# Kernel tuning notes

Measured on AMD Instinct MI355X. Metric: run time of the kernel, lower is better.

## Reference

```python
import jax, jax.numpy as jnp
import numpy as np


def topk_sparsify(x, k):
    # keep k entries with largest |x|, zero the rest (matches TopKFunction.forward)
    _, idx = jax.lax.top_k(jnp.abs(x), k)            # [B, k]
    vals = jnp.take_along_axis(x, idx, axis=-1)      # [B, k]
    out = jnp.zeros_like(x)
    b = jnp.arange(x.shape[0])[:, None]              # [B, 1]
    return out.at[b, idx].set(vals)


def setup_inputs() -> dict:
    key = jax.random.key(0)
    k1, k2, k3 = jax.random.split(key, 3)
    B, D, L = 4096, 768, 16384
    x = jax.random.normal(k1, (B, D), dtype=jnp.float32)
    # kaiming_normal_(fan_out) -> std = sqrt(2 / latent_dim); then *= 2.0
    enc_w = jax.random.normal(k2, (L, D), dtype=jnp.float32) * (2.0 * np.sqrt(2.0 / L))
    enc_b = jnp.zeros((L,), dtype=jnp.float32)
    # torch Linear default init: uniform(-1/sqrt(fan_in), 1/sqrt(fan_in))
    bound = 1.0 / np.sqrt(L)
    dec_w = jax.random.uniform(k3, (D, L), dtype=jnp.float32, minval=-bound, maxval=bound)
    dec_b = jnp.zeros((D,), dtype=jnp.float32)
    return {"x": x, "enc_w": enc_w, "enc_b": enc_b, "dec_w": dec_w, "dec_b": dec_b, "k": 32}


def reference(x, enc_w, enc_b, dec_w, dec_b, k):
    pre = x @ enc_w.T + enc_b            # [B, L]
    latents = topk_sparsify(pre, k)      # [B, L], k-sparse per row
    recon = latents @ dec_w.T + dec_b    # [B, D]
    return (recon, latents, pre)
```

## Files before the change

kernel.cpp:

```cpp
#include <hip/hip_runtime.h>
#include <hip/hip_bf16.h>
#include <stdint.h>


typedef __attribute__((ext_vector_type(8))) short bf16x8;
typedef __attribute__((ext_vector_type(4))) float f32x4;

__device__ __forceinline__ ushort f2bf_rne(float v) {
    unsigned u = __float_as_uint(v);
    return (ushort)((u + 0x7fffu + ((u >> 16) & 1u)) >> 16);
}
__device__ __forceinline__ float bf2f(ushort h) {
    return __uint_as_float(((unsigned)h) << 16);
}

__global__ __launch_bounds__(256)
void pack_bf16(const float* __restrict__ X, ushort* __restrict__ Ph,
               int R16KT, int KT, int K)
{
    int t = blockIdx.x * 256 + threadIdx.x;
    if (t >= R16KT * 64) return;
    int lane = t & 63;
    int rest = t >> 6;
    int r16 = rest / KT, kt = rest - r16 * KT;
    int row = (r16 << 4) + (lane & 15);
    int k0  = (kt << 5) + ((lane >> 4) << 3);
    const float* src = X + (size_t)row * K + k0;

    uint hw[4];
    #pragma unroll
    for (int i = 0; i < 4; ++i) {
        float v0 = src[2 * i], v1 = src[2 * i + 1];
        hw[i] = (uint)f2bf_rne(v0) | ((uint)f2bf_rne(v1) << 16);
    }
    *reinterpret_cast<uint4*>(Ph + (size_t)t * 8) = make_uint4(hw[0], hw[1], hw[2], hw[3]);
}

__global__ __launch_bounds__(256, 2)
void encoder_mfma1(const ushort* __restrict__ Ah, const ushort* __restrict__ Wh,
                   const float* __restrict__ bias, float* __restrict__ C,
                   int M, int N, int K)
{
    __shared__ ushort lds[8192];
    const int KT = K >> 5;
    const int tid  = threadIdx.x;
    const int lane = tid & 63;
    const int wid  = tid >> 6;

    int nwg  = gridDim.x;
    int flat = blockIdx.x;
    int cpx  = nwg >> 3;
    int swz  = (flat & 7) * cpx + (flat >> 3);
    const int gx = N >> 7;
    const int bx = swz % gx, by = swz / gx;

    const int wr = wid >> 1, wc = wid & 1;

    f32x4 acc[4][4];
    #pragma unroll
    for (int m = 0; m < 4; ++m)
        #pragma unroll
        for (int n = 0; n < 4; ++n) acc[m][n] = (f32x4){0.f, 0.f, 0.f, 0.f};

    for (int kt = 0; kt < KT; ++kt) {
        #pragma unroll
        for (int c0 = 0; c0 < 4; ++c0) {
            int c   = (wid << 2) + c0;
            int fr  = c & 7;
            int rb  = ((c < 8) ? (by << 3) : (bx << 3)) + fr;
            const ushort* g = ((c < 8) ? Ah : Wh) + (((size_t)rb * KT + kt) * 64 + lane) * 8;
            ushort* dst = &lds[c * 512];
            __builtin_amdgcn_global_load_lds(
                (const __attribute__((address_space(1))) unsigned int*)g,
                (__attribute__((address_space(3))) unsigned int*)dst, 16, 0, 0);
        }
        __syncthreads();

        bf16x8 ah[4], bh[4];
        #pragma unroll
        for (int m = 0; m < 4; ++m)
            ah[m] = *reinterpret_cast<const bf16x8*>(&lds[((wr << 2) + m) * 512 + lane * 8]);
        #pragma unroll
        for (int n = 0; n < 4; ++n)
            bh[n] = *reinterpret_cast<const bf16x8*>(&lds[4096 + ((wc << 2) + n) * 512 + lane * 8]);

        #pragma unroll
        for (int m = 0; m < 4; ++m)
            #pragma unroll
            for (int n = 0; n < 4; ++n)
                acc[m][n] = __builtin_amdgcn_mfma_f32_16x16x32_bf16(ah[m], bh[n], acc[m][n], 0, 0, 0);
        __syncthreads();
    }

    const int r_in = (lane >> 4) << 2;
    const int c_in = lane & 15;
    #pragma unroll
    for (int n = 0; n < 4; ++n) {
        const int gc = (bx << 7) + (wc << 6) + (n << 4) + c_in;
        const float bv = bias[gc];
        #pragma unroll
        for (int m = 0; m < 4; ++m) {
            const int gr0 = (by << 7) + (wr << 6) + (m << 4) + r_in;
            #pragma unroll
            for (int q = 0; q < 4; ++q)
                C[(size_t)(gr0 + q) * N + gc] = acc[m][n][q] + bv;
        }
    }
}

#define SR_CAP 1024
#define SR_ZCAP 128

__global__ __launch_bounds__(256, 8)
void select_refine(const float* __restrict__ pre, const float* __restrict__ x,
                   const float* __restrict__ enc_w, const float* __restrict__ enc_b,
                   float* __restrict__ latents, int* __restrict__ sel_idx,
                   float* __restrict__ sel_val, const int* __restrict__ kptr,
                   int D, int L)
{
    const int b   = blockIdx.x;
    const int tid = threadIdx.x;
    const float* row = pre + (size_t)b * L;
    float* lrow = latents + (size_t)b * L;

    __shared__ float    xs[768];
    __shared__ float    smp[256];
    __shared__ float    sthr[3];
    __shared__ int      cnt;
    __shared__ unsigned long long lkey[SR_CAP];
    __shared__ float    lval[SR_CAP];
    __shared__ float    s_tk;
    __shared__ float    s_xn2;
    __shared__ int      zidx[SR_ZCAP];
    __shared__ float    zval[SR_ZCAP];
    __shared__ int      zn;
    __shared__ int      fin_n;
    __shared__ int      fin_i[64];
    __shared__ float    fin_v[64];
    __shared__ float    red[4];

    int k = *kptr; if (k > 64) k = 64; if (k < 1) k = 1;

    float xn2p = 0.f;
    for (int i = tid; i < D; i += 256) {
        float v = x[(size_t)b * D + i];
        xs[i] = v;
        xn2p = fmaf(v, v, xn2p);
    }
    #pragma unroll
    for (int off = 32; off > 0; off >>= 1) xn2p += __shfl_down(xn2p, off);
    if ((tid & 63) == 0) red[tid >> 6] = xn2p;
    if (tid == 0) { zn = 0; fin_n = 0; }
    __syncthreads();
    if (tid == 0) s_xn2 = red[0] + red[1] + red[2] + red[3];

    const int stride = L >> 8;
    smp[tid] = fabsf(row[(size_t)tid * stride]);
    __syncthreads();
    {
        float s = smp[tid];
        int r = 0;
        for (int j = 0; j < 256; ++j) {
            float o = smp[j];
            r += (o > s || (o == s && j < tid)) ? 1 : 0;
        }
        if (r == 1) sthr[0] = s;
        if (r == 3) sthr[1] = s;
        if (r == 7) sthr[2] = s;
    }
    __syncthreads();

    float t = sthr[1];
    int n = 0;
    for (int attempt = 0; attempt < 2; ++attempt) {
        __syncthreads();
        if (tid == 0) cnt = 0;
        __syncthreads();
        for (int i = tid * 4; i < L; i += 1024) {
            float4 v = *reinterpret_cast<const float4*>(row + i);
            float vv[4] = {v.x, v.y, v.z, v.w};
            #pragma unroll
            for (int j = 0; j < 4; ++j) {
                float av = fabsf(vv[j]);
                if (av >= t) {
                    int p = atomicAdd(&cnt, 1);
                    if (p < SR_CAP) {
                        lkey[p] = ((unsigned long long)__float_as_uint(av) << 32)
                                  | (unsigned)(~(i + j));
                        lval[p] = vv[j];
                    }
                }
            }
        }
        __syncthreads();
        n = cnt;
        if (n >= 48 && n <= SR_CAP) break;
        t = (n < 48) ? sthr[2] : sthr[0];
    }
    if (n > SR_CAP) n = SR_CAP;
    if (k > n) k = n;

    const float4 z4 = make_float4(0.f, 0.f, 0.f, 0.f);
    for (int i = tid * 4; i < L; i += 1024)
        *reinterpret_cast<float4*>(lrow + i) = z4;

    for (int i = tid; i < n; i += 256) {
        unsigned long long ki = lkey[i];
        int rk = 0;
        for (int j = 0; j < n; ++j) rk += (lkey[j] > ki) ? 1 : 0;
        if (rk == k - 1) s_tk = fabsf(lval[i]);
    }
    __syncthreads();

    const float tk = s_tk;
    const float m  = 1.2e-3f * sqrtf(s_xn2);

    for (int i = tid; i < n; i += 256) {
        float a = fabsf(lval[i]);
        if (a > tk + m) {
            int p = atomicAdd(&fin_n, 1);
            fin_i[p] = (int)(~(unsigned)lkey[i]);
            fin_v[p] = lval[i];
        } else if (a >= tk - m) {
            int zp = atomicAdd(&zn, 1);
            if (zp < SR_ZCAP) zidx[zp] = (int)(~(unsigned)lkey[i]);
        }
    }
    __syncthreads();
    const int A  = fin_n;
    const int nz = (zn < SR_ZCAP) ? zn : SR_ZCAP;

    for (int z = 0; z < nz; ++z) {
        const int l = zidx[z];
        const float* wrow = enc_w + (size_t)l * D;
        float s = 0.f;
        for (int d = tid; d < D; d += 256) s = fmaf(xs[d], wrow[d], s);
        #pragma unroll
        for (int off = 32; off > 0; off >>= 1) s += __shfl_down(s, off);
        if ((tid & 63) == 0) red[tid >> 6] = s;
        __syncthreads();
        if (tid == 0) zval[z] = red[0] + red[1] + red[2] + red[3] + enc_b[l];
        __syncthreads();
    }

    const int k2 = k - A;
    if (tid < nz) {
        float az = fabsf(zval[tid]);
        int   iz = zidx[tid];
        int rz = 0;
        for (int j = 0; j < nz; ++j) {
            float aj = fabsf(zval[j]);
            rz += (aj > az || (aj == az && zidx[j] < iz)) ? 1 : 0;
        }
        if (rz < k2) {
            int p = atomicAdd(&fin_n, 1);
            if (p < 64) { fin_i[p] = iz; fin_v[p] = zval[tid]; }
        }
    }
    __syncthreads();

    int fn = fin_n; if (fn > 64) fn = 64;
    if (tid < fn) {
        float av = fabsf(fin_v[tid]);
        int   ii = fin_i[tid];
        int fr = 0;
        for (int j = 0; j < fn; ++j) {
            float aj = fabsf(fin_v[j]);
            fr += (aj > av || (aj == av && fin_i[j] < ii)) ? 1 : 0;
        }
        sel_idx[(size_t)b * 64 + fr] = ii;
        sel_val[(size_t)b * 64 + fr] = fin_v[tid];
        lrow[ii] = fin_v[tid];
    }
    if (tid >= fn && tid < k) {
        sel_idx[(size_t)b * 64 + tid] = 0;
        sel_val[(size_t)b * 64 + tid] = 0.f;
    }
}

__global__ void transpose_bf16(const float* __restrict__ W, ushort* __restrict__ WT,
                               int D, int L)
{
    __shared__ float tile[32][33];
    const int l0 = blockIdx.x * 32;
    const int d0 = blockIdx.y * 32;
    const int tx = threadIdx.x;
    const int ty = threadIdx.y;
    for (int i = ty; i < 32; i += 8)
        tile[i][tx] = W[(size_t)(d0 + i) * L + (l0 + tx)];
    __syncthreads();
    for (int i = ty; i < 32; i += 8)
        WT[(size_t)(l0 + i) * D + (d0 + tx)] = f2bf_rne(tile[tx][i]);
}

__global__ __launch_bounds__(256)
void decoder_selb(const int* __restrict__ sel_idx, const float* __restrict__ sel_val,
                  const ushort* __restrict__ WT, const float* __restrict__ dbias,
                  float* __restrict__ recon, const int* __restrict__ kptr, int D)
{
    const int b = blockIdx.x;
    const int tid = threadIdx.x;
    int k = *kptr; if (k > 64) k = 64; if (k < 1) k = 1;
    __shared__ int   si[64];
    __shared__ float sv[64];
    if (tid < k) { si[tid] = sel_idx[(size_t)b * 64 + tid]; sv[tid] = sel_val[(size_t)b * 64 + tid]; }
    __syncthreads();
    float a0 = 0.f, a1 = 0.f, a2 = 0.f;
    for (int j = 0; j < k; ++j) {
        const ushort* w = WT + (size_t)si[j] * D;
        const float v = sv[j];
        if (tid < D)        a0 = fmaf(v, bf2f(w[tid]),       a0);
        if (tid + 256 < D)  a1 = fmaf(v, bf2f(w[tid + 256]), a1);
        if (tid + 512 < D)  a2 = fmaf(v, bf2f(w[tid + 512]), a2);
    }
    if (tid < D)       recon[(size_t)b * D + tid]       = a0 + dbias[tid];
    if (tid + 256 < D) recon[(size_t)b * D + tid + 256] = a1 + dbias[tid + 256];
    if (tid + 512 < D) recon[(size_t)b * D + tid + 512] = a2 + dbias[tid + 512];
}

#define BM 128
#define BN 128
#define BKT 16

__global__ __launch_bounds__(256, 2)
void encoder_gemm(const float* __restrict__ A, const float* __restrict__ Bw,
                  const float* __restrict__ bias, float* __restrict__ C,
                  int M, int N, int K)
{
    __shared__ float As[BKT][BM + 4];
    __shared__ float Bs[BKT][BN + 4];
    const int tid  = threadIdx.x;
    const int row0 = blockIdx.y * BM;
    const int col0 = blockIdx.x * BN;
    const int lrow = tid >> 2;
    const int lc4  = (tid & 3) * 4;
    const int ty = tid >> 4;
    const int tx = tid & 15;
    float acc[2][2][4][4];
    #pragma unroll
    for (int a = 0; a < 2; ++a)
        #pragma unroll
        for (int b = 0; b < 2; ++b)
            #pragma unroll
            for (int i = 0; i < 4; ++i)
                #pragma unroll
                for (int j = 0; j < 4; ++j) acc[a][b][i][j] = 0.f;
    for (int k0 = 0; k0 < K; k0 += BKT) {
        float4 a0 = *reinterpret_cast<const float4*>(A + (size_t)(row0 + lrow)      * K + k0 + lc4);
        float4 a1 = *reinterpret_cast<const float4*>(A + (size_t)(row0 + lrow + 64) * K + k0 + lc4);
        float4 b0 = *reinterpret_cast<const float4*>(Bw + (size_t)(col0 + lrow)      * K + k0 + lc4);
        float4 b1 = *reinterpret_cast<const float4*>(Bw + (size_t)(col0 + lrow + 64) * K + k0 + lc4);
        __syncthreads();
        As[lc4 + 0][lrow] = a0.x; As[lc4 + 1][lrow] = a0.y;
        As[lc4 + 2][lrow] = a0.z; As[lc4 + 3][lrow] = a0.w;
        As[lc4 + 0][lrow + 64] = a1.x; As[lc4 + 1][lrow + 64] = a1.y;
        As[lc4 + 2][lrow + 64] = a1.z; As[lc4 + 3][lrow + 64] = a1.w;
        Bs[lc4 + 0][lrow] = b0.x; Bs[lc4 + 1][lrow] = b0.y;
        Bs[lc4 + 2][lrow] = b0.z; Bs[lc4 + 3][lrow] = b0.w;
        Bs[lc4 + 0][lrow + 64] = b1.x; Bs[lc4 + 1][lrow + 64] = b1.y;
        Bs[lc4 + 2][lrow + 64] = b1.z; Bs[lc4 + 3][lrow + 64] = b1.w;
        __syncthreads();
        #pragma unroll
        for (int kk = 0; kk < BKT; ++kk) {
            float av[2][4], bv[2][4];
            *reinterpret_cast<float4*>(av[0]) = *reinterpret_cast<const float4*>(&As[kk][ty * 4]);
            *reinterpret_cast<float4*>(av[1]) = *reinterpret_cast<const float4*>(&As[kk][ty * 4 + 64]);
            *reinterpret_cast<float4*>(bv[0]) = *reinterpret_cast<const float4*>(&Bs[kk][tx * 4]);
            *reinterpret_cast<float4*>(bv[1]) = *reinterpret_cast<const float4*>(&Bs[kk][tx * 4 + 64]);
            #pragma unroll
            for (int a = 0; a < 2; ++a)
                #pragma unroll
                for (int i = 0; i < 4; ++i)
                    #pragma unroll
                    for (int b = 0; b < 2; ++b)
                        #pragma unroll
                        for (int j = 0; j < 4; ++j)
                            acc[a][b][i][j] = fmaf(av[a][i], bv[b][j], acc[a][b][i][j]);
        }
    }
    #pragma unroll
    for (int a = 0; a < 2; ++a)
        #pragma unroll
        for (int i = 0; i < 4; ++i) {
            const int r = row0 + a * 64 + ty * 4 + i;
            #pragma unroll
            for (int b = 0; b < 2; ++b) {
                const int c = col0 + b * 64 + tx * 4;
                float4 o;
                o.x = acc[a][b][i][0] + bias[c + 0];
                o.y = acc[a][b][i][1] + bias[c + 1];
                o.z = acc[a][b][i][2] + bias[c + 2];
                o.w = acc[a][b][i][3] + bias[c + 3];
                *reinterpret_cast<float4*>(C + (size_t)r * N + c) = o;
            }
        }
}

__global__ __launch_bounds__(256)
void topk_kernel(const float* __restrict__ pre, float* __restrict__ latents,
                 const int* __restrict__ kptr, int L)
{
    const int b   = blockIdx.x;
    const int tid = threadIdx.x;
    int k = *kptr; if (k > 64) k = 64; if (k < 1) k = 1;
    const float* row = pre + (size_t)b * L;
    __shared__ unsigned hist[2048];
    __shared__ unsigned coarse[256];
    __shared__ unsigned sh_cgt, sh_prefix;
    __shared__ int      tie_n;
    __shared__ int      tie_idx[1024];
    __shared__ float    tie_val[1024];
    unsigned cgt = 0, prefix = 0;
    for (int level = 0; level < 3; ++level) {
        const int nb     = (level == 0) ? 2048 : 1024;
        const int shift  = (level == 0) ? 20 : (level == 1 ? 10 : 0);
        const int pshift = (level == 1) ? 20 : 10;
        for (int i = tid; i < nb; i += 256) hist[i] = 0;
        __syncthreads();
        for (int i = tid * 4; i < L; i += 1024) {
            float4 v = *reinterpret_cast<const float4*>(row + i);
            float vv[4] = {v.x, v.y, v.z, v.w};
            #pragma unroll
            for (int j = 0; j < 4; ++j) {
                unsigned key = __float_as_uint(vv[j]) & 0x7fffffffu;
                if (level == 0 || (key >> pshift) == prefix)
                    atomicAdd(&hist[(key >> shift) & (nb - 1)], 1u);
            }
        }
        __syncthreads();
        const int per = nb / 256;
        unsigned s = 0;
        for (int j = 0; j < per; ++j) s += hist[tid * per + j];
        coarse[tid] = s;
        __syncthreads();
        if (tid == 0) {
            unsigned run = cgt;
            int bin = 0;
            for (int c = 255; c >= 0; --c) {
                if (run + coarse[c] >= (unsigned)k) {
                    bin = c * per + per - 1;
                    for (; bin > c * per; --bin) {
                        if (run + hist[bin] >= (unsigned)k) break;
                        run += hist[bin];
                    }
                    break;
                }
                run += coarse[c];
            }
            sh_cgt = run;
            sh_prefix = (level == 0) ? (unsigned)bin : ((prefix << 10) | (unsigned)bin);
        }
        __syncthreads();
        cgt = sh_cgt; prefix = sh_prefix;
        __syncthreads();
    }
    const unsigned T = prefix;
    const int r = k - (int)cgt;
    if (tid == 0) tie_n = 0;
    __syncthreads();
    float* lrow = latents + (size_t)b * L;
    for (int i = tid * 4; i < L; i += 1024) {
        float4 v = *reinterpret_cast<const float4*>(row + i);
        float vv[4] = {v.x, v.y, v.z, v.w};
        #pragma unroll
        for (int j = 0; j < 4; ++j) {
            unsigned key = __float_as_uint(vv[j]) & 0x7fffffffu;
            if (key > T) {
                lrow[i + j] = vv[j];
            } else if (key == T) {
                int p = atomicAdd(&tie_n, 1);
                if (p < 1024) { tie_idx[p] = i + j; tie_val[p] = vv[j]; }
            }
        }
    }
    __syncthreads();
    if (tid == 0) {
        int nn = tie_n; if (nn > 1024) nn = 1024;
        for (int a = 1; a < nn; ++a) {
            int ia = tie_idx[a]; float va = tie_val[a];
            int c = a - 1;
            while (c >= 0 && tie_idx[c] > ia) {
                tie_idx[c + 1] = tie_idx[c]; tie_val[c + 1] = tie_val[c]; --c;
            }
            tie_idx[c + 1] = ia; tie_val[c + 1] = va;
        }
        int take = r < nn ? r : nn;
        for (int a = 0; a < take; ++a) lrow[tie_idx[a]] = tie_val[a];
    }
}

__global__ void transpose_kernel(const float* __restrict__ W, float* __restrict__ WT,
                                 int D, int L)
{
    __shared__ float tile[32][33];
    const int l0 = blockIdx.x * 32;
    const int d0 = blockIdx.y * 32;
    const int tx = threadIdx.x;
    const int ty = threadIdx.y;
    for (int i = ty; i < 32; i += 8)
        tile[i][tx] = W[(size_t)(d0 + i) * L + (l0 + tx)];
    __syncthreads();
    for (int i = ty; i < 32; i += 8)
        WT[(size_t)(l0 + i) * D + (d0 + tx)] = tile[tx][i];
}

__global__ __launch_bounds__(256)
void decoder_kernel(const float* __restrict__ latents, const float* __restrict__ WT,
                    const float* __restrict__ Wfall, const float* __restrict__ dbias,
                    float* __restrict__ recon, int L, int D, int useWT)
{
    const int b = blockIdx.x;
    const int tid = threadIdx.x;
    __shared__ int   nsel;
    __shared__ int   s_idx[64];
    __shared__ float s_val[64];
    if (tid == 0) nsel = 0;
    __syncthreads();
    const float* lrow = latents + (size_t)b * L;
    for (int i = tid * 4; i < L; i += 1024) {
        float4 v = *reinterpret_cast<const float4*>(lrow + i);
        float vv[4] = {v.x, v.y, v.z, v.w};
        #pragma unroll
        for (int j = 0; j < 4; ++j) {
            if (vv[j] != 0.0f) {
                int p = atomicAdd(&nsel, 1);
                if (p < 64) { s_idx[p] = i + j; s_val[p] = vv[j]; }
            }
        }
    }
    __syncthreads();
    if (tid == 0) {
        int n = nsel; if (n > 64) n = 64;
        for (int a = 1; a < n; ++a) {
            int ia = s_idx[a]; float va = s_val[a];
            int c = a - 1;
            while (c >= 0 && s_idx[c] > ia) {
                s_idx[c + 1] = s_idx[c]; s_val[c + 1] = s_val[c]; --c;
            }
            s_idx[c + 1] = ia; s_val[c + 1] = va;
        }
    }
    __syncthreads();
    int n = nsel; if (n > 64) n = 64;
    float accv[3] = {0.f, 0.f, 0.f};
    if (useWT) {
        for (int j = 0; j < n; ++j) {
            const int l = s_idx[j]; const float v = s_val[j];
            const float* w = WT + (size_t)l * D;
            #pragma unroll
            for (int c = 0; c < 3; ++c) {
                int d = tid + c * 256;
                if (d < D) accv[c] = fmaf(v, w[d], accv[c]);
            }
        }
    } else {
        for (int j = 0; j < n; ++j) {
            const int l = s_idx[j]; const float v = s_val[j];
            #pragma unroll
            for (int c = 0; c < 3; ++c) {
                int d = tid + c * 256;
                if (d < D) accv[c] = fmaf(v, Wfall[(size_t)d * L + l], accv[c]);
            }
        }
    }
    #pragma unroll
    for (int c = 0; c < 3; ++c) {
        int d = tid + c * 256;
        if (d < D) recon[(size_t)b * D + d] = accv[c] + dbias[d];
    }
}

extern "C" void kernel_launch(void* const* d_in, const int* in_sizes, int n_in,
                              void* d_out, int out_size, void* d_ws, size_t ws_size,
                              hipStream_t stream)
{
    const float* x     = (const float*)d_in[0];
    const float* enc_w = (const float*)d_in[1];
    const float* enc_b = (const float*)d_in[2];
    const float* dec_w = (const float*)d_in[3];
    const float* dec_b = (const float*)d_in[4];
    const int*   kptr  = (const int*)d_in[5];

    const int D = in_sizes[4];
    const int L = in_sizes[2];
    const int B = in_sizes[0] / D;

    float* recon   = (float*)d_out;
    float* latents = recon + (size_t)B * D;
    float* pre     = latents + (size_t)B * L;

    const size_t szA  = (size_t)B * D * 2;
    const size_t szW  = (size_t)L * D * 2;
    const size_t szSel = (size_t)B * 64 * 4;
    size_t off = 0;
    ushort* Ah  = (ushort*)((char*)d_ws + off); off += szA;
    ushort* Wh  = (ushort*)((char*)d_ws + off); off += szW;
    ushort* WTb = (ushort*)((char*)d_ws + off); off += szW;
    int*    sidx = (int*)((char*)d_ws + off);   off += szSel;
    float*  sval = (float*)((char*)d_ws + off); off += szSel;
    const size_t need = off;

    const bool shapes_ok = (B % 128 == 0) && (L % 1024 == 0) && (L >= 2048) &&
                           (D % 32 == 0) && (D <= 768) &&
                           (((size_t)(B / 128) * (L / 128)) % 8 == 0);
    const bool fast = shapes_ok && ws_size >= need;

    if (fast) {
        const int KT = D / 32;
        int totA = (B / 16) * KT * 64;
        pack_bf16<<<(totA + 255) / 256, 256, 0, stream>>>(x, Ah, (B / 16) * KT, KT, D);
        int totW = (L / 16) * KT * 64;
        pack_bf16<<<(totW + 255) / 256, 256, 0, stream>>>(enc_w, Wh, (L / 16) * KT, KT, D);
        transpose_bf16<<<dim3(L / 32, D / 32), dim3(32, 8), 0, stream>>>(dec_w, WTb, D, L);
        encoder_mfma1<<<(B / 128) * (L / 128), 256, 0, stream>>>(Ah, Wh, enc_b, pre, B, L, D);
        select_refine<<<B, 256, 0, stream>>>(pre, x, enc_w, enc_b, latents, sidx, sval, kptr, D, L);
        decoder_selb<<<B, 256, 0, stream>>>(sidx, sval, WTb, dec_b, recon, kptr, D);
    } else {
        hipMemsetAsync(latents, 0, (size_t)B * L * sizeof(float), stream);
        int useWT = 0;
        const size_t szWT = (size_t)L * D * 4;
        if (ws_size >= szWT) {
            useWT = 1;
            transpose_kernel<<<dim3(L / 32, D / 32), dim3(32, 8), 0, stream>>>(dec_w, (float*)d_ws, D, L);
        }
        encoder_gemm<<<dim3(L / BN, B / BM), 256, 0, stream>>>(x, enc_w, enc_b, pre, B, L, D);
        topk_kernel<<<B, 256, 0, stream>>>(pre, latents, kptr, L);
        decoder_kernel<<<B, 256, 0, stream>>>(latents, (float*)d_ws, dec_w, dec_b, recon, L, D, useWT);
    }
}
```

Baseline: 532.9 us.

## Fuse top-k candidate collection and latent zeroing into encoder GEMM epilogue

The encoder epilogue now writes zeros to the latents tile and, for each output whose magnitude exceeds a per-row statistical threshold, appends it to a per-row candidate list via global atomics. The threshold comes from the squared norm of the encoder weights, accumulated in the pack kernel, and the row norm of x. The select kernel reads this small candidate list instead of rescanning the full pre row and zeroing latents itself, falling back to the old sampling scan when the list is too small, too large or the k-th value is too close to the threshold. This removes a full re-read of pre and a separate latents write pass, at the cost of global atomics and scattered writes in the GEMM epilogue plus two extra memsets and a small kernel.

```diff
diff --git a/kernel.cpp b/kernel.cpp
--- a/kernel.cpp
+++ b/kernel.cpp
@@ -6,6 +6,8 @@
 typedef __attribute__((ext_vector_type(8))) short bf16x8;
 typedef __attribute__((ext_vector_type(4))) float f32x4;
 
+#define CAND_CAP 512
+
 __device__ __forceinline__ ushort f2bf_rne(float v) {
     unsigned u = __float_as_uint(v);
     return (ushort)((u + 0x7fffu + ((u >> 16) & 1u)) >> 16);
@@ -16,7 +18,7 @@
 
 __global__ __launch_bounds__(256)
 void pack_bf16(const float* __restrict__ X, ushort* __restrict__ Ph,
-               int R16KT, int KT, int K)
+               float* __restrict__ ss, int R16KT, int KT, int K)
 {
     int t = blockIdx.x * 256 + threadIdx.x;
     if (t >= R16KT * 64) return;
@@ -28,20 +30,45 @@
     const float* src = X + (size_t)row * K + k0;
 
     uint hw[4];
+    float sq = 0.f;
     #pragma unroll
     for (int i = 0; i < 4; ++i) {
         float v0 = src[2 * i], v1 = src[2 * i + 1];
+        sq = fmaf(v0, v0, sq); sq = fmaf(v1, v1, sq);
         hw[i] = (uint)f2bf_rne(v0) | ((uint)f2bf_rne(v1) << 16);
     }
     *reinterpret_cast<uint4*>(Ph + (size_t)t * 8) = make_uint4(hw[0], hw[1], hw[2], hw[3]);
+    if (ss) {
+        #pragma unroll
+        for (int off = 32; off > 0; off >>= 1) sq += __shfl_down(sq, off);
+        if (lane == 0) atomicAdd(ss, sq);
+    }
+}
+
+__global__ __launch_bounds__(256)
+void row_thr(const float* __restrict__ x, const float* __restrict__ ss,
+             float* __restrict__ thr, int D, int LD_total)
+{
+    int row  = blockIdx.x * 4 + (threadIdx.x >> 6);
+    int lane = threadIdx.x & 63;
+    const float* xr = x + (size_t)row * D;
+    float s = 0.f;
+    for (int d = lane; d < D; d += 64) { float v = xr[d]; s = fmaf(v, v, s); }
+    #pragma unroll
+    for (int off = 32; off > 0; off >>= 1) s += __shfl_down(s, off);
+    if (lane == 0)
+        thr[row] = 2.5f * sqrtf(ss[0] / (float)LD_total) * sqrtf(s);
 }
 
 __global__ __launch_bounds__(256, 2)
 void encoder_mfma1(const ushort* __restrict__ Ah, const ushort* __restrict__ Wh,
                    const float* __restrict__ bias, float* __restrict__ C,
+                   float* __restrict__ Lat, uint2* __restrict__ cand,
+                   int* __restrict__ cnt, const float* __restrict__ thr,
                    int M, int N, int K)
 {
     __shared__ ushort lds[8192];
+    __shared__ float  thr_s[128];
     const int KT = K >> 5;
     const int tid  = threadIdx.x;
     const int lane = tid & 63;
@@ -55,6 +82,8 @@
     const int bx = swz % gx, by = swz / gx;
 
     const int wr = wid >> 1, wc = wid & 1;
+
+    if (tid < 128) thr_s[tid] = thr[(by << 7) + tid];
 
     f32x4 acc[4][4];
     #pragma unroll
@@ -100,10 +129,21 @@
         const float bv = bias[gc];
         #pragma unroll
         for (int m = 0; m < 4; ++m) {
-            const int gr0 = (by << 7) + (wr << 6) + (m << 4) + r_in;
+            const int lr0 = (wr << 6) + (m << 4) + r_in;
             #pragma unroll
-            for (int q = 0; q < 4; ++q)
-                C[(size_t)(gr0 + q) * N + gc] = acc[m][n][q] + bv;
+            for (int q = 0; q < 4; ++q) {
+                const int lr = lr0 + q;
+                const int gr = (by << 7) + lr;
+                const float v = acc[m][n][q] + bv;
+                C[(size_t)gr * N + gc]   = v;
+                Lat[(size_t)gr * N + gc] = 0.0f;
+                if (fabsf(v) >= thr_s[lr]) {
+                    int p = atomicAdd(&cnt[gr], 1);
+                    if (p < CAND_CAP)
+                        cand[(size_t)gr * CAND_CAP + p] =
+                            make_uint2((unsigned)gc, __float_as_uint(v));
+                }
+            }
         }
     }
 }
@@ -114,6 +154,8 @@
 __global__ __launch_bounds__(256, 8)
 void select_refine(const float* __restrict__ pre, const float* __restrict__ x,
                    const float* __restrict__ enc_w, const float* __restrict__ enc_b,
+                   const uint2* __restrict__ cand, const int* __restrict__ cnt,
+                   const float* __restrict__ thr,
                    float* __restrict__ latents, int* __restrict__ sel_idx,
                    float* __restrict__ sel_val, const int* __restrict__ kptr,
                    int D, int L)
@@ -126,7 +168,7 @@
     __shared__ float    xs[768];
     __shared__ float    smp[256];
     __shared__ float    sthr[3];
-    __shared__ int      cnt;
+    __shared__ int      scnt;
     __shared__ unsigned long long lkey[SR_CAP];
     __shared__ float    lval[SR_CAP];
     __shared__ float    s_tk;
@@ -154,66 +196,88 @@
     __syncthreads();
     if (tid == 0) s_xn2 = red[0] + red[1] + red[2] + red[3];
 
-    const int stride = L >> 8;
-    smp[tid] = fabsf(row[(size_t)tid * stride]);
-    __syncthreads();
-    {
-        float s = smp[tid];
-        int r = 0;
-        for (int j = 0; j < 256; ++j) {
-            float o = smp[j];
-            r += (o > s || (o == s && j < tid)) ? 1 : 0;
-        }
-        if (r == 1) sthr[0] = s;
-        if (r == 3) sthr[1] = s;
-        if (r == 7) sthr[2] = s;
-    }
-    __syncthreads();
-
-    float t = sthr[1];
+    const int nc = cnt[b];
+    bool usecand = (nc >= k && nc <= CAND_CAP);
     int n = 0;
-    for (int attempt = 0; attempt < 2; ++attempt) {
-        __syncthreads();
-        if (tid == 0) cnt = 0;
-        __syncthreads();
-        for (int i = tid * 4; i < L; i += 1024) {
-            float4 v = *reinterpret_cast<const float4*>(row + i);
-            float vv[4] = {v.x, v.y, v.z, v.w};
-            #pragma unroll
-            for (int j = 0; j < 4; ++j) {
-                float av = fabsf(vv[j]);
-                if (av >= t) {
-                    int p = atomicAdd(&cnt, 1);
-                    if (p < SR_CAP) {
-                        lkey[p] = ((unsigned long long)__float_as_uint(av) << 32)
-                                  | (unsigned)(~(i + j));
-                        lval[p] = vv[j];
+    if (usecand) {
+        for (int i = tid; i < nc; i += 256) {
+            uint2 e = cand[(size_t)b * CAND_CAP + i];
+            lval[i] = __uint_as_float(e.y);
+            lkey[i] = ((unsigned long long)(e.y & 0x7fffffffu) << 32)
+                      | (unsigned)(~e.x);
+        }
+        n = nc;
+    }
+    __syncthreads();
+
+    const float mm   = 1.2e-3f * sqrtf(s_xn2);
+    const float thrb = thr[b];
+    int kk = 0;
+
+    for (int pass = 0; pass < 2; ++pass) {
+        if (!usecand) {
+            const int stride = L >> 8;
+            smp[tid] = fabsf(row[(size_t)tid * stride]);
+            __syncthreads();
+            {
+                float s = smp[tid];
+                int r = 0;
+                for (int j = 0; j < 256; ++j) {
+                    float o = smp[j];
+                    r += (o > s || (o == s && j < tid)) ? 1 : 0;
+                }
+                if (r == 1) sthr[0] = s;
+                if (r == 3) sthr[1] = s;
+                if (r == 7) sthr[2] = s;
+            }
+            __syncthreads();
+            float t = sthr[1];
+            for (int attempt = 0; attempt < 2; ++attempt) {
+                __syncthreads();
+                if (tid == 0) scnt = 0;
+                __syncthreads();
+                for (int i = tid * 4; i < L; i += 1024) {
+                    float4 v = *reinterpret_cast<const float4*>(row + i);
+                    float vv[4] = {v.x, v.y, v.z, v.w};
+                    #pragma unroll
+                    for (int j = 0; j < 4; ++j) {
+                        float av = fabsf(vv[j]);
+                        if (av >= t) {
+                            int p = atomicAdd(&scnt, 1);
+                            if (p < SR_CAP) {
+                                lkey[p] = ((unsigned long long)__float_as_uint(av) << 32)
+                                          | (unsigned)(~(i + j));
+                                lval[p] = vv[j];
+                            }
+                        }
                     }
                 }
-            }
-        }
-        __syncthreads();
-        n = cnt;
-        if (n >= 48 && n <= SR_CAP) break;
-        t = (n < 48) ? sthr[2] : sthr[0];
-    }
-    if (n > SR_CAP) n = SR_CAP;
-    if (k > n) k = n;
-
-    const float4 z4 = make_float4(0.f, 0.f, 0.f, 0.f);
-    for (int i = tid * 4; i < L; i += 1024)
-        *reinterpret_cast<float4*>(lrow + i) = z4;
-
-    for (int i = tid; i < n; i += 256) {
-        unsigned long long ki = lkey[i];
-        int rk = 0;
-        for (int j = 0; j < n; ++j) rk += (lkey[j] > ki) ? 1 : 0;
-        if (rk == k - 1) s_tk = fabsf(lval[i]);
-    }
-    __syncthreads();
-
+                __syncthreads();
+                n = scnt;
+                if (n >= 48 && n <= SR_CAP) break;
+                t = (n < 48) ? sthr[2] : sthr[0];
+            }
+            if (n > SR_CAP) n = SR_CAP;
+        }
+        kk = (k < n) ? k : n;
+
+        if (tid == 0) s_tk = 0.f;
+        __syncthreads();
+        for (int i = tid; i < n; i += 256) {
+            unsigned long long ki = lkey[i];
+            int rk = 0;
+            for (int j = 0; j < n; ++j) rk += (lkey[j] > ki) ? 1 : 0;
+            if (rk == kk - 1) s_tk = fabsf(lval[i]);
+        }
+        __syncthreads();
+
+        if (!usecand) break;
+        if (s_tk >= thrb + 2.0f * mm) break;
+        usecand = false;
+    }
+    k = kk;
     const float tk = s_tk;
-    const float m  = 1.2e-3f * sqrtf(s_xn2);
+    const float m  = mm;
 
     for (int i = tid; i < n; i += 256) {
         float a = fabsf(lval[i]);
@@ -589,15 +653,19 @@
     float* latents = recon + (size_t)B * D;
     float* pre     = latents + (size_t)B * L;
 
-    const size_t szA  = (size_t)B * D * 2;
-    const size_t szW  = (size_t)L * D * 2;
+    const size_t szA   = (size_t)B * D * 2;
+    const size_t szW   = (size_t)L * D * 2;
     const size_t szSel = (size_t)B * 64 * 4;
     size_t off = 0;
-    ushort* Ah  = (ushort*)((char*)d_ws + off); off += szA;
-    ushort* Wh  = (ushort*)((char*)d_ws + off); off += szW;
-    ushort* WTb = (ushort*)((char*)d_ws + off); off += szW;
-    int*    sidx = (int*)((char*)d_ws + off);   off += szSel;
-    float*  sval = (float*)((char*)d_ws + off); off += szSel;
+    ushort* Ah   = (ushort*)((char*)d_ws + off); off += szA;
+    ushort* Wh   = (ushort*)((char*)d_ws + off); off += szW;
+    ushort* WTb  = (ushort*)((char*)d_ws + off); off += szW;
+    int*    sidx = (int*)((char*)d_ws + off);    off += szSel;
+    float*  sval = (float*)((char*)d_ws + off);  off += szSel;
+    uint2*  candb = (uint2*)((char*)d_ws + off); off += (size_t)B * CAND_CAP * 8;
+    int*    cntb  = (int*)((char*)d_ws + off);   off += (size_t)B * 4;
+    float*  thrb  = (float*)((char*)d_ws + off); off += (size_t)B * 4;
+    float*  ssb   = (float*)((char*)d_ws + off); off += 256;
     const size_t need = off;
 
     const bool shapes_ok = (B % 128 == 0) && (L % 1024 == 0) && (L >= 2048) &&
@@ -607,13 +675,18 @@
 
     if (fast) {
         const int KT = D / 32;
+        hipMemsetAsync(cntb, 0, (size_t)B * 4, stream);
+        hipMemsetAsync(ssb, 0, 4, stream);
         int totA = (B / 16) * KT * 64;
-        pack_bf16<<<(totA + 255) / 256, 256, 0, stream>>>(x, Ah, (B / 16) * KT, KT, D);
+        pack_bf16<<<(totA + 255) / 256, 256, 0, stream>>>(x, Ah, nullptr, (B / 16) * KT, KT, D);
         int totW = (L / 16) * KT * 64;
-        pack_bf16<<<(totW + 255) / 256, 256, 0, stream>>>(enc_w, Wh, (L / 16) * KT, KT, D);
+        pack_bf16<<<(totW + 255) / 256, 256, 0, stream>>>(enc_w, Wh, ssb, (L / 16) * KT, KT, D);
         transpose_bf16<<<dim3(L / 32, D / 32), dim3(32, 8), 0, stream>>>(dec_w, WTb, D, L);
-        encoder_mfma1<<<(B / 128) * (L / 128), 256, 0, stream>>>(Ah, Wh, enc_b, pre, B, L, D);
-        select_refine<<<B, 256, 0, stream>>>(pre, x, enc_w, enc_b, latents, sidx, sval, kptr, D, L);
+        row_thr<<<B / 4, 256, 0, stream>>>(x, ssb, thrb, D, L * D);
+        encoder_mfma1<<<(B / 128) * (L / 128), 256, 0, stream>>>(
+            Ah, Wh, enc_b, pre, latents, candb, cntb, thrb, B, L, D);
+        select_refine<<<B, 256, 0, stream>>>(
+            pre, x, enc_w, enc_b, candb, cntb, thrb, latents, sidx, sval, kptr, D, L);
         decoder_selb<<<B, 256, 0, stream>>>(sidx, sval, WTb, dec_b, recon, kptr, D);
     } else {
         hipMemsetAsync(latents, 0, (size_t)B * L * sizeof(float), stream);
```

Result: slower. 1.080 ms (+102.7%).
